# Kernel tuning notes

Hardware: AMD Instinct MI355X
Metric: run time of the kernel (lower is better)

## Reference

```python
import jax, jax.numpy as jnp
import numpy as np
import math

B, T, C, E, H = 16, 256, 6, 512, 8


def setup_inputs() -> dict:
    key = jax.random.key(0)
    ks = jax.random.split(key, 5)
    std = 0.02
    return {
        "x": jax.random.normal(ks[0], (B, T, C, E), dtype=jnp.float32),
        "Wq": jax.random.normal(ks[1], (E, E), dtype=jnp.float32) * std,
        "bq": jnp.zeros((E,), dtype=jnp.float32),
        "Wk": jax.random.normal(ks[2], (E, E), dtype=jnp.float32) * std,
        "bk": jnp.zeros((E,), dtype=jnp.float32),
        "Wv": jax.random.normal(ks[3], (E, E), dtype=jnp.float32) * std,
        "bv": jnp.zeros((E,), dtype=jnp.float32),
        "Wp": jax.random.normal(ks[4], (E, E), dtype=jnp.float32) * std,
        "bp": jnp.zeros((E,), dtype=jnp.float32),
    }


def reference(x, Wq, bq, Wk, bk, Wv, bv, Wp, bp):
    b, t, c, e = x.shape
    hd = e // H
    # nn.Linear: y = x @ W^T + b, then view(B,T,C,H,hd).transpose(1,3) -> (B,H,C,T,hd)
    def heads(W, bias):
        y = jnp.einsum('btce,fe->btcf', x, W) + bias
        return y.reshape(b, t, c, H, hd).transpose(0, 3, 2, 1, 4)  # B,H,C,T,hd

    q = heads(Wq, bq)
    k = heads(Wk, bk)
    v = heads(Wv, bv)

    scale = 1.0 / math.sqrt(hd)
    att = jnp.einsum('bhctd,bhcsd->bhcts', q, k) * scale  # B,H,C,T,T
    causal = jnp.tril(jnp.ones((t, t), dtype=bool))
    att = jnp.where(causal, att, -jnp.inf)
    att = jax.nn.softmax(att, axis=-1)

    y = jnp.einsum('bhcts,bhcsd->bhctd', att, v)  # B,H,C,T,hd
    # permute(0,3,1,2,4) -> (B,T,H,C,hd), then view(B,T,C,E) (faithful to torch)
    y = y.transpose(0, 3, 1, 2, 4).reshape(b, t, c, e)
    return jnp.einsum('btce,fe->btcf', y, Wp) + bp
```

## Files before the change

### kernel.cpp

```cpp
#include <hip/hip_runtime.h>


typedef unsigned short u16;
typedef short bf16x8 __attribute__((ext_vector_type(8)));
typedef float f32x4 __attribute__((ext_vector_type(4)));
typedef u16 u16x4 __attribute__((ext_vector_type(4)));

#define MFMA16(a, b, c) __builtin_amdgcn_mfma_f32_16x16x32_bf16((a), (b), (c), 0, 0, 0)

__device__ __forceinline__ u16 f2b(float f) {
  union { float f; unsigned u; } v; v.f = f;
  unsigned r = v.u + 0x7fffu + ((v.u >> 16) & 1u);
  return (u16)(r >> 16);
}
__device__ __forceinline__ void gl_lds16(const void* g, void* l) {
  __builtin_amdgcn_global_load_lds(
      (const __attribute__((address_space(1))) void*)g,
      (__attribute__((address_space(3))) void*)l, 16, 0, 0);
}

__global__ void cvt_w(const float* W0, const float* W1, const float* W2,
                      const float* W3, u16* dst) {
  const float* src = (blockIdx.y == 0) ? W0 : (blockIdx.y == 1) ? W1
                   : (blockIdx.y == 2) ? W2 : W3;
  const int idx = (blockIdx.x * 256 + threadIdx.x) * 4;
  f32x4 v = *(const f32x4*)(src + idx);
  u16x4 o; o.x = f2b(v.x); o.y = f2b(v.y); o.z = f2b(v.z); o.w = f2b(v.w);
  *(u16x4*)(dst + (size_t)blockIdx.y * 262144 + idx) = o;
}

__global__ void cvt_x(const float* __restrict__ src, u16* __restrict__ dst) {
  const size_t idx = ((size_t)blockIdx.x * 256 + threadIdx.x) * 4;
  f32x4 v = *(const f32x4*)(src + idx);
  u16x4 o; o.x = f2b(v.x); o.y = f2b(v.y); o.z = f2b(v.z); o.w = f2b(v.w);
  *(u16x4*)(dst + idx) = o;
}

#define STAGE(k, bi) do { \
  _Pragma("unroll") \
  for (int j_ = 0; j_ < 4; ++j_) \
    if (j_ < 3 || tid < 256) \
      gl_lds16(gsrc[j_] + (k) * 64, Sb + (bi) * 28672 + fl[j_]); \
} while (0)

__global__ __launch_bounds__(512, 2) void qkv_attn(
    const u16* __restrict__ xbf, const u16* __restrict__ wbf,
    const float* __restrict__ bq, const float* __restrict__ bk,
    const float* __restrict__ bv, u16* __restrict__ y_ws)
{
  const int blk = blockIdx.x;
  const int b   = blk / 48;
  const int h   = (blk / 6) % 8;
  const int c   = blk % 6;

  __shared__ u16 LDS[28672];
  char* Ksb  = (char*)LDS;
  char* Vtsb = (char*)LDS + 16384;
  char* Sb   = (char*)LDS;

  const int tid  = threadIdx.x;
  const int lane = tid & 63;
  const int wv   = tid >> 6;
  const int r    = lane & 15;
  const int qd   = lane >> 4;
  const int tiles[2] = { wv, 15 - wv };
  char* Qw = (char*)LDS + 32768 + wv * 2048;

  const char* gsrc[4]; int fl[4];
  #pragma unroll
  for (int j = 0; j < 4; ++j) {
    const int idx  = j * 512 + tid;
    const int flat = idx * 16;
    const int row  = flat >> 6;
    const int gc   = (((flat >> 4) & 3) - (row >> 1)) & 3;
    fl[j] = flat;
    if (row < 256) {
      gsrc[j] = (const char*)xbf +
                ((size_t)(b * 256 + row) * 6 + c) * 1024 + gc * 16;
    } else {
      const int wr  = row - 256;
      const int tau = (wr >> 6) & 3;
      const int n   = wr & 63;
      gsrc[j] = (const char*)wbf + (size_t)tau * 524288 +
                (size_t)(h * 64 + n) * 1024 + gc * 16;
    }
  }

  int aoff[2], boff[3][4];
  #pragma unroll
  for (int ti = 0; ti < 2; ++ti) {
    const int row = tiles[ti] * 16 + r;
    aoff[ti] = row * 64 + ((qd + (row >> 1)) & 3) * 16;
  }
  #pragma unroll
  for (int tau = 0; tau < 3; ++tau)
    #pragma unroll
    for (int nt = 0; nt < 4; ++nt) {
      const int row = 256 + tau * 64 + nt * 16 + r;
      boff[tau][nt] = row * 64 + ((qd + (row >> 1)) & 3) * 16;
    }

  f32x4 acc[3][2][4] = {};

  STAGE(0, 0);
  __syncthreads();

  #pragma unroll 2
  for (int kt = 0; kt < 16; ++kt) {
    const int bi = kt & 1;
    if (kt < 15) STAGE(kt + 1, bi ^ 1);

    bf16x8 af[2], bfr[3][4];
    #pragma unroll
    for (int ti = 0; ti < 2; ++ti)
      af[ti] = *(const bf16x8*)(Sb + bi * 28672 + aoff[ti]);
    #pragma unroll
    for (int tau = 0; tau < 3; ++tau)
      #pragma unroll
      for (int nt = 0; nt < 4; ++nt)
        bfr[tau][nt] = *(const bf16x8*)(Sb + bi * 28672 + boff[tau][nt]);

    #pragma unroll
    for (int tau = 0; tau < 3; ++tau)
      #pragma unroll
      for (int ti = 0; ti < 2; ++ti)
        #pragma unroll
        for (int nt = 0; nt < 4; ++nt)
          acc[tau][ti][nt] = MFMA16(af[ti], bfr[tau][nt], acc[tau][ti][nt]);

    __syncthreads();
  }

  float bqv[4], bkv[4], bvv[4];
  #pragma unroll
  for (int nt = 0; nt < 4; ++nt) {
    const int col = h * 64 + nt * 16 + r;
    bqv[nt] = bq[col]; bkv[nt] = bk[col]; bvv[nt] = bv[col];
  }

  const int lo0 = ( qd      ^ (r & 7)) << 4;
  const int lo1 = ((4 + qd) ^ (r & 7)) << 4;

  f32x4 o_acc[2][4] = {};
  float l_acc[2][4] = {{0.f,0.f,0.f,0.f},{0.f,0.f,0.f,0.f}};

  #pragma unroll
  for (int sc = 0; sc < 2; ++sc) {
    if (sc) __syncthreads();

    #pragma unroll
    for (int nt = 0; nt < 4; ++nt)
      #pragma unroll
      for (int rr = 0; rr < 4; ++rr) {
        const int tl = tiles[sc] * 16 + qd * 4 + rr - sc * 128;
        const int kb = tl * 128 +
            (((nt * 2 + (r >> 3)) ^ (tl & 7)) << 4) + (r & 7) * 2;
        *(u16*)(Ksb + kb) = f2b(acc[1][sc][nt][rr] + bkv[nt]);
        const int vb = (nt * 16 + r) * 256 +
            (((tl >> 3) ^ (r & 7)) << 4) + (tl & 7) * 2;
        *(u16*)(Vtsb + vb) = f2b(acc[2][sc][nt][rr] + bvv[nt]);
      }
    __syncthreads();

    #pragma unroll
    for (int ti = 0; ti < 2; ++ti) {
      if (sc == 1 && ti == 0) continue;
      const int mt  = tiles[ti];
      const int i0  = mt * 16;
      const int nch = (mt >> 2) + 1;

      #pragma unroll
      for (int nt = 0; nt < 4; ++nt)
        #pragma unroll
        for (int rr = 0; rr < 4; ++rr) {
          const int prow = qd * 4 + rr;
          const int qb = prow * 128 +
              (((nt * 2 + (r >> 3)) ^ (prow & 7)) << 4) + (r & 7) * 2;
          *(u16*)(Qw + qb) = f2b(acc[0][ti][nt][rr] + bqv[nt]);
        }
      asm volatile("s_waitcnt lgkmcnt(0)" ::: "memory");

      bf16x8 qf[2];
      qf[0] = *(const bf16x8*)(Qw + r * 128 + lo0);
      qf[1] = *(const bf16x8*)(Qw + r * 128 + lo1);
      asm volatile("s_waitcnt lgkmcnt(0)" ::: "memory");

      #pragma unroll
      for (int jcl = 0; jcl < 2; ++jcl) {
        const int jcg = sc * 2 + jcl;
        if (jcg >= nch) continue;
        const int j0l = jcl * 64;
        const int j0g = jcg * 64;

        f32x4 s[4] = {};
        #pragma unroll
        for (int nt = 0; nt < 4; ++nt) {
          const int krow = j0l + nt * 16 + r;
          bf16x8 kf0 = *(const bf16x8*)(Ksb + krow * 128 + lo0);
          s[nt] = MFMA16(qf[0], kf0, s[nt]);
          bf16x8 kf1 = *(const bf16x8*)(Ksb + krow * 128 + lo1);
          s[nt] = MFMA16(qf[1], kf1, s[nt]);
        }

        #pragma unroll
        for (int nt = 0; nt < 4; ++nt)
          #pragma unroll
          for (int rr = 0; rr < 4; ++rr) {
            const int i = i0 + qd * 4 + rr;
            const int j = j0g + nt * 16 + r;
            float p = __builtin_exp2f(fminf(s[nt][rr], 500.f) *
                                      0.1803368801111244f);
            if (j > i) p = 0.f;
            l_acc[ti][rr] += p;
            const int prow = qd * 4 + rr;
            const int pb = prow * 128 +
                (((nt * 2 + (r >> 3)) ^ (prow & 7)) << 4) + (r & 7) * 2;
            *(u16*)(Qw + pb) = f2b(p);
          }
        asm volatile("s_waitcnt lgkmcnt(0)" ::: "memory");

        bf16x8 pf[2];
        pf[0] = *(const bf16x8*)(Qw + r * 128 + lo0);
        pf[1] = *(const bf16x8*)(Qw + r * 128 + lo1);
        #pragma unroll
        for (int ntd = 0; ntd < 4; ++ntd) {
          const int vrow = ntd * 16 + r;
          bf16x8 vf0 = *(const bf16x8*)(Vtsb + vrow * 256 +
              ((((j0l >> 3) + qd) ^ (r & 7)) << 4));
          o_acc[ti][ntd] = MFMA16(pf[0], vf0, o_acc[ti][ntd]);
          bf16x8 vf1 = *(const bf16x8*)(Vtsb + vrow * 256 +
              ((((j0l >> 3) + 4 + qd) ^ (r & 7)) << 4));
          o_acc[ti][ntd] = MFMA16(pf[1], vf1, o_acc[ti][ntd]);
        }
      }
    }
  }

  const size_t obase = ((size_t)b * 256) * 3072 + h * 384 + c * 64;
  #pragma unroll
  for (int ti = 0; ti < 2; ++ti) {
    const int i0 = tiles[ti] * 16;
    float linv[4];
    #pragma unroll
    for (int rr = 0; rr < 4; ++rr) {
      float sum = l_acc[ti][rr];
      sum += __shfl_xor(sum, 1, 16);
      sum += __shfl_xor(sum, 2, 16);
      sum += __shfl_xor(sum, 4, 16);
      sum += __shfl_xor(sum, 8, 16);
      linv[rr] = 1.f / sum;
    }
    #pragma unroll
    for (int ntd = 0; ntd < 4; ++ntd)
      #pragma unroll
      for (int rr = 0; rr < 4; ++rr) {
        const int t = i0 + qd * 4 + rr;
        const int d = ntd * 16 + r;
        y_ws[obase + (size_t)t * 3072 + d] = f2b(o_acc[ti][ntd][rr] * linv[rr]);
      }
  }
}

__global__ __launch_bounds__(256, 3) void gemm_bt(
    const u16* __restrict__ A,
    const u16* W0, const u16* W1, const u16* W2,
    const float* bs0, const float* bs1, const float* bs2,
    u16* O0, u16* O1, u16* O2,
    float* OF,
    int qkv_mode)
{
  const int z = blockIdx.z;
  const u16* W    = (z == 0) ? W0 : (z == 1) ? W1 : W2;
  const float* bs = (z == 0) ? bs0 : (z == 1) ? bs1 : bs2;
  u16* O          = (z == 0) ? O0 : (z == 1) ? O1 : O2;

  const int m0 = blockIdx.x * 128;
  const int n0 = blockIdx.y * 128;

  __shared__ u16 As[128 * 32];
  __shared__ u16 Bs[128 * 32];

  const int tid  = threadIdx.x;
  const int lane = tid & 63;
  const int wv   = tid >> 6;
  const int r    = lane & 15;
  const int qd   = lane >> 4;
  const int wm   = (wv & 1) * 64;
  const int wn   = (wv >> 1) * 64;

  f32x4 acc[4][4] = {};

  for (int k0 = 0; k0 < 512; k0 += 32) {
    __syncthreads();
    #pragma unroll
    for (int it = 0; it < 2; ++it) {
      const int flat = (it * 256 + tid) * 16;
      const int row  = flat >> 6;
      const int swc  = (flat >> 4) & 3;
      const int gc   = (swc - (row >> 1)) & 3;
      gl_lds16((const char*)A + (size_t)(m0 + row) * 1024 + k0 * 2 + gc * 16,
               (char*)As + flat);
      gl_lds16((const char*)W + (size_t)(n0 + row) * 1024 + k0 * 2 + gc * 16,
               (char*)Bs + flat);
    }
    __syncthreads();

    bf16x8 af[4], bf[4];
    #pragma unroll
    for (int mt = 0; mt < 4; ++mt) {
      const int row = wm + mt * 16 + r;
      const int sw  = (qd + (row >> 1)) & 3;
      af[mt] = *(const bf16x8*)((const char*)As + row * 64 + sw * 16);
    }
    #pragma unroll
    for (int nt = 0; nt < 4; ++nt) {
      const int row = wn + nt * 16 + r;
      const int sw  = (qd + (row >> 1)) & 3;
      bf[nt] = *(const bf16x8*)((const char*)Bs + row * 64 + sw * 16);
    }
    #pragma unroll
    for (int mt = 0; mt < 4; ++mt)
      #pragma unroll
      for (int nt = 0; nt < 4; ++nt)
        acc[mt][nt] = MFMA16(af[mt], bf[nt], acc[mt][nt]);
  }

  float bv[4];
  #pragma unroll
  for (int nt = 0; nt < 4; ++nt) bv[nt] = bs[n0 + wn + nt * 16 + r];

  if (qkv_mode) {
    #pragma unroll
    for (int mt = 0; mt < 4; ++mt) {
      #pragma unroll
      for (int rr = 0; rr < 4; ++rr) {
        const int m   = m0 + wm + mt * 16 + qd * 4 + rr;
        const int b   = m / 1536;
        const int rem = m - b * 1536;
        const int t   = rem / 6;
        const int c   = rem - t * 6;
        #pragma unroll
        for (int nt = 0; nt < 4; ++nt) {
          const int f = n0 + wn + nt * 16 + r;
          const int hh = f >> 6;
          const int d = f & 63;
          const size_t addr = ((((size_t)b * 8 + hh) * 6 + c) * 256 + t) * 64 + d;
          O[addr] = f2b(acc[mt][nt][rr] + bv[nt]);
        }
      }
    }
  } else {
    #pragma unroll
    for (int mt = 0; mt < 4; ++mt) {
      #pragma unroll
      for (int rr = 0; rr < 4; ++rr) {
        const int m = m0 + wm + mt * 16 + qd * 4 + rr;
        #pragma unroll
        for (int nt = 0; nt < 4; ++nt) {
          const int f = n0 + wn + nt * 16 + r;
          OF[(size_t)m * 512 + f] = acc[mt][nt][rr] + bv[nt];
        }
      }
    }
  }
}

extern "C" void kernel_launch(void* const* d_in, const int* in_sizes, int n_in,
                              void* d_out, int out_size, void* d_ws, size_t ws_size,
                              hipStream_t stream) {
  const float* x  = (const float*)d_in[0];
  const float* Wq = (const float*)d_in[1];
  const float* bq = (const float*)d_in[2];
  const float* Wk = (const float*)d_in[3];
  const float* bk = (const float*)d_in[4];
  const float* Wv = (const float*)d_in[5];
  const float* bv = (const float*)d_in[6];
  const float* Wp = (const float*)d_in[7];
  const float* bp = (const float*)d_in[8];
  float* out = (float*)d_out;

  const size_t PER_B = 256 * 6 * 512;
  const size_t WSEG  = 4 * 262144;

  int NB = 16;
  while (NB > 1 && (WSEG + (size_t)2 * NB * PER_B) * 2 > ws_size) NB >>= 1;

  u16* wbf = (u16*)d_ws;
  u16* Wpb = wbf + 3 * 262144;

  const size_t slab = (size_t)NB * PER_B;
  u16* xbf  = wbf + WSEG;
  u16* y_ws = xbf + slab;

  cvt_w<<<dim3(256, 4), 256, 0, stream>>>(Wq, Wk, Wv, Wp, wbf);

  const int nslab = 16 / NB;
  for (int s = 0; s < nslab; ++s) {
    const float* x_s  = x   + (size_t)s * NB * PER_B;
    float*      out_s = out + (size_t)s * NB * PER_B;
    cvt_x<<<dim3(NB * 768), 256, 0, stream>>>(x_s, xbf);
    qkv_attn<<<dim3(NB * 48), 512, 0, stream>>>(xbf, wbf, bq, bk, bv, y_ws);
    gemm_bt<<<dim3(NB * 12, 4, 1), 256, 0, stream>>>(
        y_ws, Wpb, Wpb, Wpb, bp, bp, bp, nullptr, nullptr, nullptr, out_s, 0);
  }
}
```

Baseline: 203.5 us.

## Triple-buffer QKV GEMM staging, merge conversion kernels, vectorize V stores

```diff
diff --git a/kernel.cpp b/kernel.cpp
--- a/kernel.cpp
+++ b/kernel.cpp
@@ -19,28 +19,32 @@
       (__attribute__((address_space(3))) void*)l, 16, 0, 0);
 }
 
-__global__ void cvt_w(const float* W0, const float* W1, const float* W2,
-                      const float* W3, u16* dst) {
-  const float* src = (blockIdx.y == 0) ? W0 : (blockIdx.y == 1) ? W1
-                   : (blockIdx.y == 2) ? W2 : W3;
-  const int idx = (blockIdx.x * 256 + threadIdx.x) * 4;
-  f32x4 v = *(const f32x4*)(src + idx);
-  u16x4 o; o.x = f2b(v.x); o.y = f2b(v.y); o.z = f2b(v.z); o.w = f2b(v.w);
-  *(u16x4*)(dst + (size_t)blockIdx.y * 262144 + idx) = o;
-}
-
-__global__ void cvt_x(const float* __restrict__ src, u16* __restrict__ dst) {
-  const size_t idx = ((size_t)blockIdx.x * 256 + threadIdx.x) * 4;
-  f32x4 v = *(const f32x4*)(src + idx);
-  u16x4 o; o.x = f2b(v.x); o.y = f2b(v.y); o.z = f2b(v.z); o.w = f2b(v.w);
-  *(u16x4*)(dst + idx) = o;
+__global__ void cvt_all(const float* __restrict__ x, u16* __restrict__ xdst,
+                        const float* W0, const float* W1, const float* W2,
+                        const float* W3, u16* __restrict__ wdst, int nxb) {
+  const int bx = blockIdx.x;
+  if (bx < nxb) {
+    const size_t idx = ((size_t)bx * 256 + threadIdx.x) * 4;
+    f32x4 v = *(const f32x4*)(x + idx);
+    u16x4 o; o.x = f2b(v.x); o.y = f2b(v.y); o.z = f2b(v.z); o.w = f2b(v.w);
+    *(u16x4*)(xdst + idx) = o;
+  } else {
+    const int wb = bx - nxb;
+    const float* src = (wb < 256) ? W0 : (wb < 512) ? W1
+                     : (wb < 768) ? W2 : W3;
+    const int idx = ((wb & 255) * 256 + threadIdx.x) * 4;
+    f32x4 v = *(const f32x4*)(src + idx);
+    u16x4 o; o.x = f2b(v.x); o.y = f2b(v.y); o.z = f2b(v.z); o.w = f2b(v.w);
+    *(u16x4*)(wdst + (size_t)(wb >> 8) * 262144 + idx) = o;
+  }
 }
 
 #define STAGE(k, bi) do { \
+  char* Sd_ = Sb + (bi) * 28672; \
   _Pragma("unroll") \
   for (int j_ = 0; j_ < 4; ++j_) \
     if (j_ < 3 || tid < 256) \
-      gl_lds16(gsrc[j_] + (k) * 64, Sb + (bi) * 28672 + fl[j_]); \
+      gl_lds16(gsrc[j_] + (k) * 64, Sd_ + fl[j_]); \
 } while (0)
 
 __global__ __launch_bounds__(512, 2) void qkv_attn(
@@ -53,7 +57,7 @@
   const int h   = (blk / 6) % 8;
   const int c   = blk % 6;
 
-  __shared__ u16 LDS[28672];
+  __shared__ u16 LDS[43008];
   char* Ksb  = (char*)LDS;
   char* Vtsb = (char*)LDS + 16384;
   char* Sb   = (char*)LDS;
@@ -103,22 +107,25 @@
   f32x4 acc[3][2][4] = {};
 
   STAGE(0, 0);
-  __syncthreads();
+  STAGE(1, 1);
 
   #pragma unroll 2
   for (int kt = 0; kt < 16; ++kt) {
-    const int bi = kt & 1;
-    if (kt < 15) STAGE(kt + 1, bi ^ 1);
-
+    if (kt < 15) { asm volatile("s_waitcnt vmcnt(3)\n\ts_barrier" ::: "memory"); }
+    else         { asm volatile("s_waitcnt vmcnt(0)\n\ts_barrier" ::: "memory"); }
+
+    if (kt + 2 < 16) STAGE(kt + 2, (kt + 2) % 3);
+
+    char* Sc = Sb + (kt % 3) * 28672;
     bf16x8 af[2], bfr[3][4];
     #pragma unroll
     for (int ti = 0; ti < 2; ++ti)
-      af[ti] = *(const bf16x8*)(Sb + bi * 28672 + aoff[ti]);
+      af[ti] = *(const bf16x8*)(Sc + aoff[ti]);
     #pragma unroll
     for (int tau = 0; tau < 3; ++tau)
       #pragma unroll
       for (int nt = 0; nt < 4; ++nt)
-        bfr[tau][nt] = *(const bf16x8*)(Sb + bi * 28672 + boff[tau][nt]);
+        bfr[tau][nt] = *(const bf16x8*)(Sc + boff[tau][nt]);
 
     #pragma unroll
     for (int tau = 0; tau < 3; ++tau)
@@ -127,9 +134,8 @@
         #pragma unroll
         for (int nt = 0; nt < 4; ++nt)
           acc[tau][ti][nt] = MFMA16(af[ti], bfr[tau][nt], acc[tau][ti][nt]);
-
-    __syncthreads();
-  }
+  }
+  __syncthreads();
 
   float bqv[4], bkv[4], bvv[4];
   #pragma unroll
@@ -148,18 +154,28 @@
   for (int sc = 0; sc < 2; ++sc) {
     if (sc) __syncthreads();
 
-    #pragma unroll
-    for (int nt = 0; nt < 4; ++nt)
-      #pragma unroll
-      for (int rr = 0; rr < 4; ++rr) {
-        const int tl = tiles[sc] * 16 + qd * 4 + rr - sc * 128;
-        const int kb = tl * 128 +
-            (((nt * 2 + (r >> 3)) ^ (tl & 7)) << 4) + (r & 7) * 2;
-        *(u16*)(Ksb + kb) = f2b(acc[1][sc][nt][rr] + bkv[nt]);
+    {
+      const int tl0 = tiles[sc] * 16 + qd * 4 - sc * 128;
+      #pragma unroll
+      for (int nt = 0; nt < 4; ++nt) {
+        u16x4 pv;
+        #pragma unroll
+        for (int rr = 0; rr < 4; ++rr)
+          ((u16*)&pv)[rr] = f2b(acc[2][sc][nt][rr] + bvv[nt]);
         const int vb = (nt * 16 + r) * 256 +
-            (((tl >> 3) ^ (r & 7)) << 4) + (tl & 7) * 2;
-        *(u16*)(Vtsb + vb) = f2b(acc[2][sc][nt][rr] + bvv[nt]);
+            (((tl0 >> 3) ^ (r & 7)) << 4) + (tl0 & 7) * 2;
+        *(u16x4*)(Vtsb + vb) = pv;
       }
+      #pragma unroll
+      for (int nt = 0; nt < 4; ++nt)
+        #pragma unroll
+        for (int rr = 0; rr < 4; ++rr) {
+          const int tl = tl0 + rr;
+          const int kb = tl * 128 +
+              (((nt * 2 + (r >> 3)) ^ (tl & 7)) << 4) + (r & 7) * 2;
+          *(u16*)(Ksb + kb) = f2b(acc[1][sc][nt][rr] + bkv[nt]);
+        }
+    }
     __syncthreads();
 
     #pragma unroll
@@ -392,13 +408,13 @@
   u16* xbf  = wbf + WSEG;
   u16* y_ws = xbf + slab;
 
-  cvt_w<<<dim3(256, 4), 256, 0, stream>>>(Wq, Wk, Wv, Wp, wbf);
-
   const int nslab = 16 / NB;
   for (int s = 0; s < nslab; ++s) {
     const float* x_s  = x   + (size_t)s * NB * PER_B;
     float*      out_s = out + (size_t)s * NB * PER_B;
-    cvt_x<<<dim3(NB * 768), 256, 0, stream>>>(x_s, xbf);
+    const int nxb = NB * 768;
+    const int grid = (s == 0) ? nxb + 1024 : nxb;
+    cvt_all<<<dim3(grid), 256, 0, stream>>>(x_s, xbf, Wq, Wk, Wv, Wp, wbf, nxb);
     qkv_attn<<<dim3(NB * 48), 512, 0, stream>>>(xbf, wbf, bq, bk, bv, y_ws);
     gemm_bt<<<dim3(NB * 12, 4, 1), 256, 0, stream>>>(
         y_ws, Wpb, Wpb, Wpb, bp, bp, bp, nullptr, nullptr, nullptr, out_s, 0);
```

After: 202.0 us. About the same (-0.7%).
